# Performance work log

Measured on AMD Instinct MI355X. Metric: run time of the kernel, lower is better.

Reference implementation:

```python
import jax, jax.numpy as jnp
import numpy as np

B, F, H, W, C = 8, 32, 224, 224, 3
L = B * F
BASE = 1.1


def _warp_basis_np():
    # Reproduces skimage ProjectiveTransform.estimate for the 4 corner tweaks
    corners = {(0, 0): (-1, 0), (0, 1): (0, 2), (1, 0): (1, -1), (1, 1): (2, 1)}
    src = list(corners)
    basis = []
    for corner, tweak in corners.items():
        dst = [tweak if s == corner else s for s in src]
        s = np.array(dst, np.float64) - 0.5  # estimate's src
        d = np.array(src, np.float64) - 0.5  # estimate's dst
        A, b = [], []
        for (x, y), (xp, yp) in zip(s, d):
            A.append([x, y, 1, 0, 0, 0, -x * xp, -y * xp]); b.append(xp)
            A.append([0, 0, 0, x, y, 1, -x * yp, -y * yp]); b.append(yp)
        h = np.linalg.solve(np.array(A), np.array(b))
        basis.append(np.append(h, 1.0).reshape(3, 3))  # H[2,2] = 1 like skimage
    return np.stack(basis).astype(np.float32)


def setup_inputs() -> dict:
    key = jax.random.key(0)
    k1, k2 = jax.random.split(key)
    x = jax.random.uniform(k1, (B, F, H, W, C), jnp.float32)
    # truncated normal in [-2,2] stddevs, mean 0, stddev 5 (matches tf truncated_normal)
    noise = jax.random.truncated_normal(k2, -2.0, 2.0, (4, 3 * L - 2), jnp.float32) * 5.0
    warp_basis = jnp.asarray(_warp_basis_np())
    return {"x": x, "noise": noise, "warp_basis": warp_basis}


def _smooth(noise_row):
    # symmetric exponential window, length 2L-1, normalized
    w = BASE ** jnp.arange(L, dtype=jnp.float32)
    w = jnp.concatenate([w[:-1], w[::-1]])
    w = w / jnp.sum(w)
    return jnp.convolve(noise_row, w, mode="valid")  # (L,) ; w symmetric so conv==corr


def _scale(sr, sc):
    return jnp.array([[sc, 0, 0], [0, sr, 0], [0, 0, 1]], jnp.float32)


def _trans(tr, tc):
    return jnp.array([[1, 0, tc], [0, 1, tr], [0, 0, 1]], jnp.float32)


def _bilinear(img, xs, ys):
    # img (H,W,C); xs,ys (H,W) source coords (x=col, y=row); zero fill outside
    h, w = img.shape[0], img.shape[1]
    x0 = jnp.floor(xs); y0 = jnp.floor(ys)
    wx = xs - x0; wy = ys - y0

    def gather(yf, xf):
        valid = (xf >= 0) & (xf <= w - 1) & (yf >= 0) & (yf <= h - 1)
        xi = jnp.clip(xf, 0, w - 1).astype(jnp.int32)
        yi = jnp.clip(yf, 0, h - 1).astype(jnp.int32)
        return img[yi, xi] * valid[..., None]

    return (gather(y0, x0) * ((1 - wy) * (1 - wx))[..., None]
            + gather(y0, x0 + 1) * ((1 - wy) * wx)[..., None]
            + gather(y0 + 1, x0) * (wy * (1 - wx))[..., None]
            + gather(y0 + 1, x0 + 1) * (wy * wx)[..., None])


def reference(x, noise, warp_basis):
    b, f, h, w, c = x.shape
    length = b * f
    vals = jax.vmap(_smooth)(noise)                 # (4, L)
    wv = jnp.maximum(vals, 0.0)[:, :, None, None]   # (4, L, 1, 1)
    eye = jnp.eye(3, dtype=jnp.float32)
    warp = jnp.sum(wv * warp_basis[:, None] + (1.0 - wv) * eye, axis=0)  # (L,3,3)
    M = (_scale(h - 1, w - 1) @ _trans(0.5, 0.5)) @ warp @ (_trans(-0.5, -0.5) @ _scale(1.0 / (h - 1), 1.0 / (w - 1)))
    imgs = x.reshape(length, h, w, c)
    rows, cols = jnp.meshgrid(jnp.arange(h, dtype=jnp.float32), jnp.arange(w, dtype=jnp.float32), indexing="ij")
    pts = jnp.stack([cols, rows, jnp.ones_like(cols)], 0)       # (3,H,W), (x,y,1)
    src = jnp.einsum("lij,jhw->lihw", M, pts)                   # (L,3,H,W)
    sx = src[:, 0] / src[:, 2]
    sy = src[:, 1] / src[:, 2]
    out = jax.vmap(_bilinear)(imgs, sx, sy)                      # (L,H,W,C)
    return out.reshape(b, f, h, w, c)
```

## Files before the change

kernel.cpp:

```cpp
#include <hip/hip_runtime.h>
#include <math.h>

#define NFRAMES 256
#define NH 224
#define NW 224
#define NPIX (NH * NW)
#define NOISE_LEN 766
#define WIN_LEN 511
#define BLOCKS_PER_FRAME (NPIX / 256)

__global__ __launch_bounds__(256) void build_mats_kernel(
    const float* __restrict__ noise,
    const float* __restrict__ basis,
    float* __restrict__ Mout) {
  __shared__ double wsh[WIN_LEN];
  __shared__ float nsh[4 * NOISE_LEN];
  __shared__ double Ssum;
  const int t = threadIdx.x;

  for (int i = t; i < 4 * NOISE_LEN; i += 256) nsh[i] = noise[i];
  for (int i = t; i < WIN_LEN; i += 256) {
    int e = 255 - abs(i - 255);
    wsh[i] = pow(1.1, (double)e);
  }
  __syncthreads();
  if (t == 0) {
    double s = 0.0;
    for (int i = 0; i < WIN_LEN; ++i) s += wsh[i];
    Ssum = s;
  }
  __syncthreads();
  const double S = Ssum;

  double wv[4];
  for (int j = 0; j < 4; ++j) {
    const float* row = nsh + j * NOISE_LEN;
    double acc = 0.0;
    for (int k = 0; k < WIN_LEN; ++k) acc = fma((double)row[t + k], wsh[k], acc);
    double v = acc / S;
    wv[j] = v > 0.0 ? v : 0.0;
  }

  double warp[9];
  const double swv = wv[0] + wv[1] + wv[2] + wv[3];
  #pragma unroll
  for (int e = 0; e < 9; ++e) {
    double acc = 0.0;
    #pragma unroll
    for (int j = 0; j < 4; ++j) acc += wv[j] * (double)basis[j * 9 + e];
    warp[e] = acc;
  }
  warp[0] += 4.0 - swv;
  warp[4] += 4.0 - swv;
  warp[8] += 4.0 - swv;

  const double W1 = (double)(NW - 1);
  const double H1 = (double)(NH - 1);
  double T[9];
  #pragma unroll
  for (int c = 0; c < 3; ++c) {
    T[0 * 3 + c] = W1 * warp[0 * 3 + c] + 0.5 * W1 * warp[2 * 3 + c];
    T[1 * 3 + c] = H1 * warp[1 * 3 + c] + 0.5 * H1 * warp[2 * 3 + c];
    T[2 * 3 + c] = warp[2 * 3 + c];
  }
  float Mo[9];
  #pragma unroll
  for (int r = 0; r < 3; ++r) {
    Mo[r * 3 + 0] = (float)(T[r * 3 + 0] / W1);
    Mo[r * 3 + 1] = (float)(T[r * 3 + 1] / H1);
    Mo[r * 3 + 2] = (float)(-0.5 * T[r * 3 + 0] - 0.5 * T[r * 3 + 1] + T[r * 3 + 2]);
  }
  #pragma unroll
  for (int e = 0; e < 9; ++e) Mout[t * 9 + e] = Mo[e];
}

__global__ __launch_bounds__(256) void warp_bilinear_kernel(
    const float* __restrict__ x,
    const float* __restrict__ M,
    float* __restrict__ out) {
  const int bid = blockIdx.x;
  const int l = bid / BLOCKS_PER_FRAME;
  const int p = (bid - l * BLOCKS_PER_FRAME) * 256 + threadIdx.x;

  const float* Mp = M + l * 9;
  const float m00 = Mp[0], m01 = Mp[1], m02 = Mp[2];
  const float m10 = Mp[3], m11 = Mp[4], m12 = Mp[5];
  const float m20 = Mp[6], m21 = Mp[7], m22 = Mp[8];

  const int r = p / NW;
  const int c = p - r * NW;
  const float cf = (float)c, rf = (float)r;

  const float fx = fmaf(m00, cf, fmaf(m01, rf, m02));
  const float fy = fmaf(m10, cf, fmaf(m11, rf, m12));
  const float fz = fmaf(m20, cf, fmaf(m21, rf, m22));
  const float inv = __builtin_amdgcn_rcpf(fz);
  const float xs = fx * inv;
  const float ys = fy * inv;

  const float x0f = floorf(xs), y0f = floorf(ys);
  const float wx = xs - x0f, wy = ys - y0f;
  const float x1f = x0f + 1.0f, y1f = y0f + 1.0f;

  const float vx0 = (x0f >= 0.0f && x0f <= (float)(NW - 1)) ? 1.0f : 0.0f;
  const float vx1 = (x1f >= 0.0f && x1f <= (float)(NW - 1)) ? 1.0f : 0.0f;
  const float vy0 = (y0f >= 0.0f && y0f <= (float)(NH - 1)) ? 1.0f : 0.0f;
  const float vy1 = (y1f >= 0.0f && y1f <= (float)(NH - 1)) ? 1.0f : 0.0f;

  const int xi0 = (int)fminf(fmaxf(x0f, 0.0f), (float)(NW - 1));
  const int xi1 = (int)fminf(fmaxf(x1f, 0.0f), (float)(NW - 1));
  const int yi0 = (int)fminf(fmaxf(y0f, 0.0f), (float)(NH - 1));
  const int yi1 = (int)fminf(fmaxf(y1f, 0.0f), (float)(NH - 1));

  const float* img = x + (size_t)l * (NPIX * 3);
  const float* p00 = img + (yi0 * NW + xi0) * 3;
  const float* p01 = img + (yi0 * NW + xi1) * 3;
  const float* p10 = img + (yi1 * NW + xi0) * 3;
  const float* p11 = img + (yi1 * NW + xi1) * 3;

  const float w00 = (1.0f - wy) * (1.0f - wx) * vy0 * vx0;
  const float w01 = (1.0f - wy) * wx * vy0 * vx1;
  const float w10 = wy * (1.0f - wx) * vy1 * vx0;
  const float w11 = wy * wx * vy1 * vx1;

  const float o0 = w00 * p00[0] + w01 * p01[0] + w10 * p10[0] + w11 * p11[0];
  const float o1 = w00 * p00[1] + w01 * p01[1] + w10 * p10[1] + w11 * p11[1];
  const float o2 = w00 * p00[2] + w01 * p01[2] + w10 * p10[2] + w11 * p11[2];

  float* op = out + ((size_t)l * NPIX + p) * 3;
  op[0] = o0;
  op[1] = o1;
  op[2] = o2;
}

extern "C" void kernel_launch(void* const* d_in, const int* in_sizes, int n_in,
                              void* d_out, int out_size, void* d_ws, size_t ws_size,
                              hipStream_t stream) {
  (void)in_sizes; (void)n_in; (void)out_size; (void)ws_size;
  const float* x     = (const float*)d_in[0];
  const float* noise = (const float*)d_in[1];
  const float* basis = (const float*)d_in[2];
  float* out  = (float*)d_out;
  float* Mbuf = (float*)d_ws;

  build_mats_kernel<<<1, 256, 0, stream>>>(noise, basis, Mbuf);
  warp_bilinear_kernel<<<NFRAMES * BLOCKS_PER_FRAME, 256, 0, stream>>>(x, Mbuf, out);
}
```

Baseline: 304.5 us.

## Parallelize matrix build across frames and use nontemporal output stores

The per-frame matrix setup kernel moves from one block doing 256 serial 511-tap double-precision convolutions per thread to 256 blocks. In each block, one wavefront per noise row splits the window and reduces it with shuffles. The window sum becomes a closed-form geometric series instead of a serial loop. The bilinear kernel's output writes become nontemporal stores to avoid polluting the cache. The setup kernel was a serial single-block prologue, so this should remove a noticeable chunk of latency. It slightly changes the rounding of the normalization constant.

```diff
diff --git a/kernel.cpp b/kernel.cpp
--- a/kernel.cpp
+++ b/kernel.cpp
@@ -9,69 +9,72 @@
 #define WIN_LEN 511
 #define BLOCKS_PER_FRAME (NPIX / 256)
 
-__global__ __launch_bounds__(256) void build_mats_kernel(
+__global__ __launch_bounds__(256) void build_mats_v2(
     const float* __restrict__ noise,
     const float* __restrict__ basis,
     float* __restrict__ Mout) {
+  const int b = blockIdx.x;
+  const int t = threadIdx.x;
+  const int j = t >> 6;
+  const int lane = t & 63;
+
   __shared__ double wsh[WIN_LEN];
-  __shared__ float nsh[4 * NOISE_LEN];
-  __shared__ double Ssum;
-  const int t = threadIdx.x;
+  __shared__ double vsh[4];
 
-  for (int i = t; i < 4 * NOISE_LEN; i += 256) nsh[i] = noise[i];
-  for (int i = t; i < WIN_LEN; i += 256) {
-    int e = 255 - abs(i - 255);
-    wsh[i] = pow(1.1, (double)e);
+  for (int k = t; k < WIN_LEN; k += 256) {
+    int e = 255 - abs(k - 255);
+    wsh[k] = pow(1.1, (double)e);
   }
   __syncthreads();
-  if (t == 0) {
-    double s = 0.0;
-    for (int i = 0; i < WIN_LEN; ++i) s += wsh[i];
-    Ssum = s;
+
+  const double S = (pow(1.1, 255.0) - 1.0) * 10.0 + (pow(1.1, 256.0) - 1.0) * 10.0;
+
+  const float* row = noise + j * NOISE_LEN + b;
+  const int k0 = lane * 8;
+  double acc = 0.0;
+  #pragma unroll
+  for (int i = 0; i < 8; ++i) {
+    const int k = k0 + i;
+    if (k < WIN_LEN) acc = fma((double)row[k], wsh[k], acc);
+  }
+  #pragma unroll
+  for (int off = 32; off > 0; off >>= 1) acc += __shfl_down(acc, off, 64);
+  if (lane == 0) {
+    const double v = acc / S;
+    vsh[j] = v > 0.0 ? v : 0.0;
   }
   __syncthreads();
-  const double S = Ssum;
 
-  double wv[4];
-  for (int j = 0; j < 4; ++j) {
-    const float* row = nsh + j * NOISE_LEN;
-    double acc = 0.0;
-    for (int k = 0; k < WIN_LEN; ++k) acc = fma((double)row[t + k], wsh[k], acc);
-    double v = acc / S;
-    wv[j] = v > 0.0 ? v : 0.0;
+  if (t == 0) {
+    const double wv0 = vsh[0], wv1 = vsh[1], wv2 = vsh[2], wv3 = vsh[3];
+    const double swv = wv0 + wv1 + wv2 + wv3;
+    double warp[9];
+    #pragma unroll
+    for (int e = 0; e < 9; ++e) {
+      warp[e] = wv0 * (double)basis[0 * 9 + e] + wv1 * (double)basis[1 * 9 + e] +
+                wv2 * (double)basis[2 * 9 + e] + wv3 * (double)basis[3 * 9 + e];
+    }
+    warp[0] += 4.0 - swv;
+    warp[4] += 4.0 - swv;
+    warp[8] += 4.0 - swv;
+
+    const double W1 = (double)(NW - 1);
+    const double H1 = (double)(NH - 1);
+    double T[9];
+    #pragma unroll
+    for (int c = 0; c < 3; ++c) {
+      T[0 * 3 + c] = W1 * warp[0 * 3 + c] + 0.5 * W1 * warp[2 * 3 + c];
+      T[1 * 3 + c] = H1 * warp[1 * 3 + c] + 0.5 * H1 * warp[2 * 3 + c];
+      T[2 * 3 + c] = warp[2 * 3 + c];
+    }
+    float* Mo = Mout + b * 9;
+    #pragma unroll
+    for (int r = 0; r < 3; ++r) {
+      Mo[r * 3 + 0] = (float)(T[r * 3 + 0] / W1);
+      Mo[r * 3 + 1] = (float)(T[r * 3 + 1] / H1);
+      Mo[r * 3 + 2] = (float)(-0.5 * T[r * 3 + 0] - 0.5 * T[r * 3 + 1] + T[r * 3 + 2]);
+    }
   }
-
-  double warp[9];
-  const double swv = wv[0] + wv[1] + wv[2] + wv[3];
-  #pragma unroll
-  for (int e = 0; e < 9; ++e) {
-    double acc = 0.0;
-    #pragma unroll
-    for (int j = 0; j < 4; ++j) acc += wv[j] * (double)basis[j * 9 + e];
-    warp[e] = acc;
-  }
-  warp[0] += 4.0 - swv;
-  warp[4] += 4.0 - swv;
-  warp[8] += 4.0 - swv;
-
-  const double W1 = (double)(NW - 1);
-  const double H1 = (double)(NH - 1);
-  double T[9];
-  #pragma unroll
-  for (int c = 0; c < 3; ++c) {
-    T[0 * 3 + c] = W1 * warp[0 * 3 + c] + 0.5 * W1 * warp[2 * 3 + c];
-    T[1 * 3 + c] = H1 * warp[1 * 3 + c] + 0.5 * H1 * warp[2 * 3 + c];
-    T[2 * 3 + c] = warp[2 * 3 + c];
-  }
-  float Mo[9];
-  #pragma unroll
-  for (int r = 0; r < 3; ++r) {
-    Mo[r * 3 + 0] = (float)(T[r * 3 + 0] / W1);
-    Mo[r * 3 + 1] = (float)(T[r * 3 + 1] / H1);
-    Mo[r * 3 + 2] = (float)(-0.5 * T[r * 3 + 0] - 0.5 * T[r * 3 + 1] + T[r * 3 + 2]);
-  }
-  #pragma unroll
-  for (int e = 0; e < 9; ++e) Mout[t * 9 + e] = Mo[e];
 }
 
 __global__ __launch_bounds__(256) void warp_bilinear_kernel(
@@ -128,9 +131,9 @@
   const float o2 = w00 * p00[2] + w01 * p01[2] + w10 * p10[2] + w11 * p11[2];
 
   float* op = out + ((size_t)l * NPIX + p) * 3;
-  op[0] = o0;
-  op[1] = o1;
-  op[2] = o2;
+  __builtin_nontemporal_store(o0, op + 0);
+  __builtin_nontemporal_store(o1, op + 1);
+  __builtin_nontemporal_store(o2, op + 2);
 }
 
 extern "C" void kernel_launch(void* const* d_in, const int* in_sizes, int n_in,
@@ -143,6 +146,6 @@
   float* out  = (float*)d_out;
   float* Mbuf = (float*)d_ws;
 
-  build_mats_kernel<<<1, 256, 0, stream>>>(noise, basis, Mbuf);
+  build_mats_v2<<<NFRAMES, 256, 0, stream>>>(noise, basis, Mbuf);
   warp_bilinear_kernel<<<NFRAMES * BLOCKS_PER_FRAME, 256, 0, stream>>>(x, Mbuf, out);
 }
```

New measurement: 264.0 us. 1.15x faster.
